# Optimization experiments

Hardware: AMD Instinct MI355X
Metric: run time of the kernel (lower is better)

Reference implementation:

```python
import jax, jax.numpy as jnp
import numpy as np

EPS = float(np.finfo(np.float32).eps)


def fake_quant_w(w):
    # per-output-channel symmetric int8 fake quant; w: (out, in)
    w_d = jax.lax.stop_gradient(w)
    max_abs = jnp.max(jnp.abs(w_d), axis=1, keepdims=True)
    scale = jnp.maximum(max_abs / 127.0, EPS)
    w_q = jnp.clip(jnp.round(w_d / scale), -127, 127)
    return w_q * scale


def woq_linear(x, w, b):
    return x @ fake_quant_w(w).T + b


def setup_inputs() -> dict:
    key = jax.random.key(0)
    ks = jax.random.split(key, 9)
    dim = 1024
    B, S = 2, 2048
    def wmat(k):
        return jax.random.normal(k, (dim, dim), dtype=jnp.float32) * (1.0 / np.sqrt(dim))
    def bvec(k):
        return jax.random.normal(k, (dim,), dtype=jnp.float32) * 0.01
    return {
        "x": jax.random.normal(ks[0], (B, S, dim), dtype=jnp.float32),
        "wq": wmat(ks[1]), "bq": bvec(ks[2]),
        "wk": wmat(ks[3]), "bk": bvec(ks[4]),
        "wv": wmat(ks[5]), "bv": bvec(ks[6]),
        "wp": wmat(ks[7]), "bp": bvec(ks[8]),
    }


def reference(x, wq, bq, wk, bk, wv, bv, wp, bp):
    B, S, C = x.shape
    H = 16
    D = C // H
    scale = D ** -0.5
    # QKV projections with fake-quantized weights -> (B, H, S, D)
    q = woq_linear(x, wq, bq).reshape(B, S, H, D).transpose(0, 2, 1, 3)
    k = woq_linear(x, wk, bk).reshape(B, S, H, D).transpose(0, 2, 1, 3)
    v = woq_linear(x, wv, bv).reshape(B, S, H, D).transpose(0, 2, 1, 3)
    attn = jnp.einsum("bhsd,bhtd->bhst", q, k) * scale  # (B,H,S,S)
    attn = jax.nn.softmax(attn, axis=-1)
    out = jnp.einsum("bhst,bhtd->bhsd", attn, v)
    out = out.transpose(0, 2, 1, 3).reshape(B, S, C)
    return woq_linear(out, wp, bp)
```

## Files before the change

kernel.cpp:

```cpp
#include <hip/hip_runtime.h>
#include <stdint.h>

typedef short bf16x8 __attribute__((ext_vector_type(8)));
typedef float f32x4 __attribute__((ext_vector_type(4)));
typedef uint16_t u16;
typedef uint32_t u32;
typedef u16 u16x4 __attribute__((ext_vector_type(4)));
typedef u32 u32x2 __attribute__((ext_vector_type(2)));
typedef u32 u32x4 __attribute__((ext_vector_type(4)));

#define EPSF 1.1920929e-07f

static __device__ __forceinline__ u16 f2bf(float f) {
  union { float f; uint32_t u; } v; v.f = f;
  return (u16)((v.u + 0x7FFFu + ((v.u >> 16) & 1u)) >> 16);
}
static __device__ __forceinline__ float bf2f(u16 h) {
  union { uint32_t u; float f; } v; v.u = ((uint32_t)h) << 16;
  return v.f;
}
static __device__ __forceinline__ float exp2_fast(float x) {
  return __builtin_amdgcn_exp2f(x);
}
static __device__ __forceinline__ u32 cvt_pk_bf16(float lo, float hi) {
  u32 r;
  asm("v_cvt_pk_bf16_f32 %0, %1, %2" : "=v"(r) : "v"(lo), "v"(hi));
  return r;
}
static __device__ __forceinline__ void gload_lds16(const void* g, void* l) {
  __builtin_amdgcn_global_load_lds(
      (const __attribute__((address_space(1))) void*)g,
      (__attribute__((address_space(3))) void*)l, 16, 0, 0);
}
template <int N>
static __device__ __forceinline__ void vmwait() {
  asm volatile("s_waitcnt vmcnt(%0)" ::"i"(N) : "memory");
}

__global__ __launch_bounds__(256) void prep_kernel(
    const float* __restrict__ wq, const float* __restrict__ wk,
    const float* __restrict__ wv, const float* __restrict__ wp,
    const float* __restrict__ x,
    u16* __restrict__ wout, float* __restrict__ scales, u16* __restrict__ xb) {
  const int t = threadIdx.x;
  if (blockIdx.x < 4096) {
    const int row = blockIdx.x & 1023;
    const int mat = blockIdx.x >> 10;
    const float* W = (mat == 0) ? wq : (mat == 1) ? wk : (mat == 2) ? wv : wp;
    const float4 v = ((const float4*)(W + (size_t)row * 1024))[t];
    float m = fmaxf(fmaxf(fabsf(v.x), fabsf(v.y)), fmaxf(fabsf(v.z), fabsf(v.w)));
#pragma unroll
    for (int off = 1; off < 64; off <<= 1) m = fmaxf(m, __shfl_xor(m, off));
    __shared__ float red[4];
    if ((t & 63) == 0) red[t >> 6] = m;
    __syncthreads();
    m = fmaxf(fmaxf(red[0], red[1]), fmaxf(red[2], red[3]));
    const float scale = fmaxf(m / 127.0f, EPSF);
    float q0 = fminf(fmaxf(rintf(v.x / scale), -127.f), 127.f);
    float q1 = fminf(fmaxf(rintf(v.y / scale), -127.f), 127.f);
    float q2 = fminf(fmaxf(rintf(v.z / scale), -127.f), 127.f);
    float q3 = fminf(fmaxf(rintf(v.w / scale), -127.f), 127.f);
    u16x4 o; o.x = f2bf(q0); o.y = f2bf(q1); o.z = f2bf(q2); o.w = f2bf(q3);
    *(u16x4*)(wout + ((size_t)(mat * 1024 + row)) * 1024 + t * 4) = o;
    if (t == 0) scales[mat * 1024 + row] = scale;
  } else {
    const int i = (blockIdx.x - 4096) * 256 + t;
    const float4 v = ((const float4*)x)[i];
    u16x4 hv;
    hv.x = f2bf(v.x); hv.y = f2bf(v.y); hv.z = f2bf(v.z); hv.w = f2bf(v.w);
    *(u16x4*)(xb + (size_t)i * 4) = hv;
  }
}

template <int MODE, int MR, int NR, int NT, int KT, int LDA>
__global__ __launch_bounds__(512) void gemm_kernel(
    const u16* __restrict__ A, const u16* __restrict__ Bw,
    const float* __restrict__ scales, const float* __restrict__ b0,
    const float* __restrict__ b1, const float* __restrict__ b2,
    u16* __restrict__ qkv, float* __restrict__ outp) {
  constexpr int BM = 2 * MR * 16;
  constexpr int BN = 4 * NR * 16;
  constexpr int OPS = BM / 64 + BN / 64;
  __shared__ u16 As[2][BM * 64];
  __shared__ u16 Bs[2][BN * 64];
  const int tid = threadIdx.x;
  const int w = tid >> 6, l = tid & 63;
  const int per = gridDim.x >> 3;
  const int L = (blockIdx.x & 7) * per + (blockIdx.x >> 3);
  const int tile_n = (L % NT) * BN;
  const int tile_m = (L / NT) * BM;
  const int wm = w >> 2, wn = w & 3;
  const int l15 = l & 15, l4 = l >> 4;
  const int sw = l15 & 7;

  f32x4 acc[MR][NR];
  const f32x4 vzero = {0.f, 0.f, 0.f, 0.f};
#pragma unroll
  for (int m = 0; m < MR; ++m)
#pragma unroll
    for (int n = 0; n < NR; ++n) acc[m][n] = vzero;

  const int r8 = tid >> 3;
  const int g = tid & 7;
  const int gs = g ^ (r8 & 7);
  auto STAGE = [&](int slot, int j) {
    const int kb = j * 64;
    const int kbB = kb & 1023;
#pragma unroll
    for (int i = 0; i < BM / 64; ++i)
      gload_lds16(A + (size_t)(tile_m + i * 64 + r8) * LDA + kb + gs * 8,
                  &As[slot][(i * 64 + r8) * 64 + g * 8]);
#pragma unroll
    for (int i = 0; i < BN / 64; ++i)
      gload_lds16(Bw + (size_t)(tile_n + i * 64 + r8) * 1024 + kbB + gs * 8,
                  &Bs[slot][(i * 64 + r8) * 64 + g * 8]);
  };

  STAGE(0, 0);
  STAGE(1, 1);
  vmwait<OPS>();
  __builtin_amdgcn_s_barrier();

  for (int j = 0; j < KT; ++j) {
    const int cur = j & 1;
#pragma unroll
    for (int ks = 0; ks < 2; ++ks) {
      bf16x8 af[MR], bfv[NR];
      const int sg8 = ((ks * 4 + l4) ^ sw) * 8;
#pragma unroll
      for (int m = 0; m < MR; ++m)
        af[m] = *(const bf16x8*)(&As[cur][(wm * (MR * 16) + m * 16 + l15) * 64 + sg8]);
#pragma unroll
      for (int n = 0; n < NR; ++n)
        bfv[n] = *(const bf16x8*)(&Bs[cur][(wn * (NR * 16) + n * 16 + l15) * 64 + sg8]);
      __builtin_amdgcn_s_setprio(1);
#pragma unroll
      for (int m = 0; m < MR; ++m)
#pragma unroll
        for (int n = 0; n < NR; ++n)
          acc[m][n] = __builtin_amdgcn_mfma_f32_16x16x32_bf16(af[m], bfv[n], acc[m][n], 0, 0, 0);
      __builtin_amdgcn_s_setprio(0);
    }
    __builtin_amdgcn_s_barrier();
    if (j + 2 < KT) {
      STAGE(cur, j + 2);
      vmwait<OPS>();
    } else {
      vmwait<0>();
    }
    __builtin_amdgcn_s_barrier();
  }

#pragma unroll
  for (int m = 0; m < MR; ++m) {
#pragma unroll
    for (int n = 0; n < NR; ++n) {
      const int col = tile_n + wn * (NR * 16) + n * 16 + l15;
      const float sc = scales[col];
      if constexpr (MODE == 0) {
        const int mat = col >> 10, oo = col & 1023;
        const float* bias = (mat == 0) ? b0 : (mat == 1) ? b1 : b2;
        const float bb = bias[oo];
        const int hh = oo >> 6, dd = oo & 63;
        if (mat == 2) {
          const int rowm0 = tile_m + wm * (MR * 16) + m * 16 + l4 * 4;
          const int b = rowm0 >> 11, s = rowm0 & 2047;
          u16x4 pk;
#pragma unroll
          for (int jj = 0; jj < 4; ++jj) pk[jj] = f2bf(acc[m][n][jj] * sc + bb);
          *(u16x4*)(qkv + (size_t)2 * 4194304 +
                    ((size_t)(b * 16 + hh) * 64 + dd) * 2048 + s) = pk;
        } else {
#pragma unroll
          for (int jj = 0; jj < 4; ++jj) {
            const int rowm = tile_m + wm * (MR * 16) + m * 16 + l4 * 4 + jj;
            const int b = rowm >> 11, s = rowm & 2047;
            float y = acc[m][n][jj] * sc + bb;
            if (mat == 0) y *= 0.18033688011112042f;
            qkv[(size_t)mat * 4194304 + ((size_t)(b * 16 + hh) * 2048 + s) * 64 + dd] = f2bf(y);
          }
        }
      } else {
        const float bb = b0[col];
#pragma unroll
        for (int jj = 0; jj < 4; ++jj) {
          const int rowm = tile_m + wm * (MR * 16) + m * 16 + l4 * 4 + jj;
          outp[(size_t)rowm * 1024 + col] = acc[m][n][jj] * sc + bb;
        }
      }
    }
  }
}

__global__ __launch_bounds__(256, 2) void attn_kernel(
    const u16* __restrict__ qg, const u16* __restrict__ kg,
    const u16* __restrict__ vtg, u16* __restrict__ po) {
  __shared__ u16 Kt[2][128 * 64];
  __shared__ u16 Vt[2][64 * 128];
  const int tid = threadIdx.x;
  const int w = tid >> 6, l = tid & 63;
  const int Lb = (blockIdx.x & 7) * 64 + (blockIdx.x >> 3);
  const int bh = Lb >> 4;
  const int qt = Lb & 15;
  const u16* qp = qg + (size_t)bh * 131072;
  const u16* kp = kg + (size_t)bh * 131072;
  const u16* vp = vtg + (size_t)bh * 131072;
  const int qrow0 = qt * 128 + w * 32;
  const int l15 = l & 15, l4 = l >> 4;
  const int sw = l15 & 7;

  auto STAGE = [&](const int slot, const int kt) {
#pragma unroll
    for (int i = 0; i < 4; ++i) {
      const int rk = i * 32 + (tid >> 3);
      gload_lds16(kp + (size_t)(kt + rk) * 64 + (((tid & 7) ^ (rk & 7)) << 3),
                  &Kt[slot][i * 2048 + tid * 8]);
    }
#pragma unroll
    for (int i = 0; i < 4; ++i) {
      const int rv = i * 16 + (tid >> 4);
      gload_lds16(vp + (size_t)rv * 2048 + kt + (((tid & 15) ^ (rv & 7)) << 3),
                  &Vt[slot][i * 2048 + tid * 8]);
    }
  };

  bf16x8 qfr[2][2];
#pragma unroll
  for (int dk = 0; dk < 2; ++dk)
#pragma unroll
    for (int qf = 0; qf < 2; ++qf)
      qfr[dk][qf] =
          *(const bf16x8*)(qp + (size_t)(qrow0 + qf * 16 + l15) * 64 + dk * 32 + l4 * 8);

  const f32x4 vzero = {0.f, 0.f, 0.f, 0.f};
  f32x4 O[4][2];
#pragma unroll
  for (int di = 0; di < 4; ++di)
#pragma unroll
    for (int qf = 0; qf < 2; ++qf) O[di][qf] = vzero;
  float lrun[2] = {0.f, 0.f};

  auto DO_ITER = [&](const int slot, const int j) {
    f32x4 sfr[2][8];
#pragma unroll
    for (int qf = 0; qf < 2; ++qf)
#pragma unroll
      for (int ki = 0; ki < 8; ++ki) sfr[qf][ki] = vzero;
#pragma unroll
    for (int dk = 0; dk < 2; ++dk) {
      bf16x8 kf[8];
#pragma unroll
      for (int ki = 0; ki < 8; ++ki)
        kf[ki] = *(const bf16x8*)(&Kt[slot][(ki * 16 + l15) * 64 + (((dk * 4 + l4) ^ sw) << 3)]);
      __builtin_amdgcn_s_setprio(1);
#pragma unroll
      for (int ki = 0; ki < 8; ++ki)
#pragma unroll
        for (int qf = 0; qf < 2; ++qf)
          sfr[qf][ki] = __builtin_amdgcn_mfma_f32_16x16x32_bf16(kf[ki], qfr[dk][qf], sfr[qf][ki], 0, 0, 0);
      __builtin_amdgcn_s_setprio(0);
    }

#pragma unroll
    for (int half = 0; half < 2; ++half) {
      u32 pw[2][8];
#pragma unroll
      for (int qf = 0; qf < 2; ++qf) {
        float rs = 0.f;
#pragma unroll
        for (int ki = 0; ki < 4; ++ki) {
          const f32x4 s4 = sfr[qf][half * 4 + ki];
          const float p0 = exp2_fast(s4[0]);
          const float p1 = exp2_fast(s4[1]);
          const float p2 = exp2_fast(s4[2]);
          const float p3 = exp2_fast(s4[3]);
          rs += (p0 + p1) + (p2 + p3);
          pw[qf][ki * 2 + 0] = cvt_pk_bf16(p0, p1);
          pw[qf][ki * 2 + 1] = cvt_pk_bf16(p2, p3);
        }
        lrun[qf] += rs;
      }

#pragma unroll
      for (int kkl = 0; kkl < 2; ++kkl) {
        const int c = half * 2 + kkl;
        const u32x4 t0 = {pw[0][kkl * 4 + 0], pw[0][kkl * 4 + 1],
                          pw[0][kkl * 4 + 2], pw[0][kkl * 4 + 3]};
        const u32x4 t1 = {pw[1][kkl * 4 + 0], pw[1][kkl * 4 + 1],
                          pw[1][kkl * 4 + 2], pw[1][kkl * 4 + 3]};
        const bf16x8 pf0 = __builtin_bit_cast(bf16x8, t0);
        const bf16x8 pf1 = __builtin_bit_cast(bf16x8, t1);
        const int o0 = (((c * 4 + (l4 >> 1)) ^ sw) << 3) + (l4 & 1) * 4;
        const int o1 = (((c * 4 + 2 + (l4 >> 1)) ^ sw) << 3) + (l4 & 1) * 4;
        bf16x8 vf[4];
#pragma unroll
        for (int di = 0; di < 4; ++di) {
          const u16* vrow = &Vt[slot][(di * 16 + l15) * 128];
          const u32x2 lo = *(const u32x2*)(vrow + o0);
          const u32x2 hi = *(const u32x2*)(vrow + o1);
          const u32x4 q = {lo.x, lo.y, hi.x, hi.y};
          vf[di] = __builtin_bit_cast(bf16x8, q);
        }
        __builtin_amdgcn_s_setprio(1);
#pragma unroll
        for (int di = 0; di < 4; ++di) {
          O[di][0] = __builtin_amdgcn_mfma_f32_16x16x32_bf16(pf0, vf[di], O[di][0], 0, 0, 0);
          O[di][1] = __builtin_amdgcn_mfma_f32_16x16x32_bf16(pf1, vf[di], O[di][1], 0, 0, 0);
        }
        __builtin_amdgcn_s_setprio(0);
      }
    }

    __builtin_amdgcn_s_barrier();
    if (j + 2 < 16) {
      STAGE(slot, (j + 2) * 128);
      vmwait<8>();
    } else {
      vmwait<0>();
    }
    __builtin_amdgcn_s_barrier();
  };

  STAGE(0, 0);
  STAGE(1, 128);
  vmwait<8>();
  __builtin_amdgcn_s_barrier();

  for (int jp = 0; jp < 8; ++jp) {
    DO_ITER(0, jp * 2);
    DO_ITER(1, jp * 2 + 1);
  }

  const int b = bh >> 4, hh = bh & 15;
#pragma unroll
  for (int qf = 0; qf < 2; ++qf) {
    lrun[qf] += __shfl_xor(lrun[qf], 16);
    lrun[qf] += __shfl_xor(lrun[qf], 32);
  }
#pragma unroll
  for (int qf = 0; qf < 2; ++qf) {
    float lq[4];
#pragma unroll
    for (int jj = 0; jj < 4; ++jj)
      lq[jj] = __builtin_amdgcn_rcpf(__shfl(lrun[qf], l4 * 4 + jj));
#pragma unroll
    for (int di = 0; di < 4; ++di)
#pragma unroll
      for (int jj = 0; jj < 4; ++jj) {
        const float oval = O[di][qf][jj] * lq[jj];
        const int srw = qrow0 + qf * 16 + l4 * 4 + jj;
        const int c = hh * 64 + di * 16 + l15;
        po[((size_t)(b * 2048 + srw)) * 1024 + c] = f2bf(oval);
      }
  }
}

extern "C" void kernel_launch(void* const* d_in, const int* in_sizes, int n_in,
                              void* d_out, int out_size, void* d_ws, size_t ws_size,
                              hipStream_t stream) {
  (void)in_sizes; (void)n_in; (void)out_size; (void)ws_size;
  const float* x  = (const float*)d_in[0];
  const float* wq = (const float*)d_in[1];
  const float* bq = (const float*)d_in[2];
  const float* wk = (const float*)d_in[3];
  const float* bk = (const float*)d_in[4];
  const float* wv = (const float*)d_in[5];
  const float* bv = (const float*)d_in[6];
  const float* wp = (const float*)d_in[7];
  const float* bp = (const float*)d_in[8];

  char* ws = (char*)d_ws;
  u16*   wquant = (u16*)ws;
  float* scales = (float*)(ws + 8388608);
  u16*   xb     = (u16*)(ws + 8404992);
  u16*   po     = xb;
  u16*   qkv    = (u16*)(ws + 25182208);

  prep_kernel<<<dim3(8192), dim3(256), 0, stream>>>(
      wq, wk, wv, wp, x, wquant, scales, xb);
  gemm_kernel<0, 4, 3, 16, 16, 1024><<<dim3(512), dim3(512), 0, stream>>>(
      xb, wquant, scales, bq, bk, bv, qkv, nullptr);
  attn_kernel<<<dim3(512), dim3(256), 0, stream>>>(
      qkv, qkv + 4194304, qkv + 8388608, po);
  gemm_kernel<1, 2, 2, 8, 16, 1024><<<dim3(512), dim3(512), 0, stream>>>(
      po, wquant + 3145728, scales + 3072, bp, nullptr, nullptr, nullptr, (float*)d_out);
}
```

Before: 96.36 us.

## Split attention KV sequence across two wave groups per block with LDS reduction

New measurement: 98.64 us. +2.4%, slower.

```diff
diff --git a/kernel.cpp b/kernel.cpp
--- a/kernel.cpp
+++ b/kernel.cpp
@@ -192,11 +192,11 @@
   }
 }
 
-__global__ __launch_bounds__(256, 2) void attn_kernel(
+__global__ __launch_bounds__(512, 4) void attn_kernel(
     const u16* __restrict__ qg, const u16* __restrict__ kg,
     const u16* __restrict__ vtg, u16* __restrict__ po) {
-  __shared__ u16 Kt[2][128 * 64];
-  __shared__ u16 Vt[2][64 * 128];
+  __shared__ u16 Kt[2][2][64 * 64];
+  __shared__ u16 Vt[2][2][64 * 64];
   const int tid = threadIdx.x;
   const int w = tid >> 6, l = tid & 63;
   const int Lb = (blockIdx.x & 7) * 64 + (blockIdx.x >> 3);
@@ -205,23 +205,19 @@
   const u16* qp = qg + (size_t)bh * 131072;
   const u16* kp = kg + (size_t)bh * 131072;
   const u16* vp = vtg + (size_t)bh * 131072;
-  const int qrow0 = qt * 128 + w * 32;
+  const int wg = w & 3, grp = w >> 2;
+  const int qrow0 = qt * 128 + wg * 32;
   const int l15 = l & 15, l4 = l >> 4;
   const int sw = l15 & 7;
 
-  auto STAGE = [&](const int slot, const int kt) {
-#pragma unroll
-    for (int i = 0; i < 4; ++i) {
-      const int rk = i * 32 + (tid >> 3);
-      gload_lds16(kp + (size_t)(kt + rk) * 64 + (((tid & 7) ^ (rk & 7)) << 3),
-                  &Kt[slot][i * 2048 + tid * 8]);
-    }
-#pragma unroll
-    for (int i = 0; i < 4; ++i) {
-      const int rv = i * 16 + (tid >> 4);
-      gload_lds16(vp + (size_t)rv * 2048 + kt + (((tid & 15) ^ (rv & 7)) << 3),
-                  &Vt[slot][i * 2048 + tid * 8]);
-    }
+  const int sr = tid >> 3, sg = tid & 7;
+  const int gsw = (sg ^ (sr & 7)) << 3;
+  auto STAGE = [&](const int slot, const int j) {
+    const int kA = j * 64, kB = 1024 + j * 64;
+    gload_lds16(kp + (size_t)(kA + sr) * 64 + gsw, &Kt[slot][0][tid * 8]);
+    gload_lds16(vp + (size_t)sr * 2048 + kA + gsw, &Vt[slot][0][tid * 8]);
+    gload_lds16(kp + (size_t)(kB + sr) * 64 + gsw, &Kt[slot][1][tid * 8]);
+    gload_lds16(vp + (size_t)sr * 2048 + kB + gsw, &Vt[slot][1][tid * 8]);
   };
 
   bf16x8 qfr[2][2];
@@ -241,80 +237,79 @@
   float lrun[2] = {0.f, 0.f};
 
   auto DO_ITER = [&](const int slot, const int j) {
-    f32x4 sfr[2][8];
+    const u16* Kb = &Kt[slot][grp][0];
+    const u16* Vb = &Vt[slot][grp][0];
+
+    f32x4 sfr[2][4];
 #pragma unroll
     for (int qf = 0; qf < 2; ++qf)
 #pragma unroll
-      for (int ki = 0; ki < 8; ++ki) sfr[qf][ki] = vzero;
+      for (int ki = 0; ki < 4; ++ki) sfr[qf][ki] = vzero;
 #pragma unroll
     for (int dk = 0; dk < 2; ++dk) {
-      bf16x8 kf[8];
-#pragma unroll
-      for (int ki = 0; ki < 8; ++ki)
-        kf[ki] = *(const bf16x8*)(&Kt[slot][(ki * 16 + l15) * 64 + (((dk * 4 + l4) ^ sw) << 3)]);
+      bf16x8 kf[4];
+#pragma unroll
+      for (int ki = 0; ki < 4; ++ki)
+        kf[ki] = *(const bf16x8*)(Kb + (ki * 16 + l15) * 64 + (((dk * 4 + l4) ^ sw) << 3));
       __builtin_amdgcn_s_setprio(1);
 #pragma unroll
-      for (int ki = 0; ki < 8; ++ki)
+      for (int ki = 0; ki < 4; ++ki)
 #pragma unroll
         for (int qf = 0; qf < 2; ++qf)
           sfr[qf][ki] = __builtin_amdgcn_mfma_f32_16x16x32_bf16(kf[ki], qfr[dk][qf], sfr[qf][ki], 0, 0, 0);
       __builtin_amdgcn_s_setprio(0);
     }
 
-#pragma unroll
-    for (int half = 0; half < 2; ++half) {
-      u32 pw[2][8];
-#pragma unroll
-      for (int qf = 0; qf < 2; ++qf) {
-        float rs = 0.f;
-#pragma unroll
-        for (int ki = 0; ki < 4; ++ki) {
-          const f32x4 s4 = sfr[qf][half * 4 + ki];
-          const float p0 = exp2_fast(s4[0]);
-          const float p1 = exp2_fast(s4[1]);
-          const float p2 = exp2_fast(s4[2]);
-          const float p3 = exp2_fast(s4[3]);
-          rs += (p0 + p1) + (p2 + p3);
-          pw[qf][ki * 2 + 0] = cvt_pk_bf16(p0, p1);
-          pw[qf][ki * 2 + 1] = cvt_pk_bf16(p2, p3);
-        }
-        lrun[qf] += rs;
+    u32 pw[2][8];
+#pragma unroll
+    for (int qf = 0; qf < 2; ++qf) {
+      float rs = 0.f;
+#pragma unroll
+      for (int ki = 0; ki < 4; ++ki) {
+        const f32x4 s4 = sfr[qf][ki];
+        const float p0 = exp2_fast(s4[0]);
+        const float p1 = exp2_fast(s4[1]);
+        const float p2 = exp2_fast(s4[2]);
+        const float p3 = exp2_fast(s4[3]);
+        rs += (p0 + p1) + (p2 + p3);
+        pw[qf][ki * 2 + 0] = cvt_pk_bf16(p0, p1);
+        pw[qf][ki * 2 + 1] = cvt_pk_bf16(p2, p3);
       }
-
-#pragma unroll
-      for (int kkl = 0; kkl < 2; ++kkl) {
-        const int c = half * 2 + kkl;
-        const u32x4 t0 = {pw[0][kkl * 4 + 0], pw[0][kkl * 4 + 1],
-                          pw[0][kkl * 4 + 2], pw[0][kkl * 4 + 3]};
-        const u32x4 t1 = {pw[1][kkl * 4 + 0], pw[1][kkl * 4 + 1],
-                          pw[1][kkl * 4 + 2], pw[1][kkl * 4 + 3]};
-        const bf16x8 pf0 = __builtin_bit_cast(bf16x8, t0);
-        const bf16x8 pf1 = __builtin_bit_cast(bf16x8, t1);
-        const int o0 = (((c * 4 + (l4 >> 1)) ^ sw) << 3) + (l4 & 1) * 4;
-        const int o1 = (((c * 4 + 2 + (l4 >> 1)) ^ sw) << 3) + (l4 & 1) * 4;
-        bf16x8 vf[4];
-#pragma unroll
-        for (int di = 0; di < 4; ++di) {
-          const u16* vrow = &Vt[slot][(di * 16 + l15) * 128];
-          const u32x2 lo = *(const u32x2*)(vrow + o0);
-          const u32x2 hi = *(const u32x2*)(vrow + o1);
-          const u32x4 q = {lo.x, lo.y, hi.x, hi.y};
-          vf[di] = __builtin_bit_cast(bf16x8, q);
-        }
-        __builtin_amdgcn_s_setprio(1);
-#pragma unroll
-        for (int di = 0; di < 4; ++di) {
-          O[di][0] = __builtin_amdgcn_mfma_f32_16x16x32_bf16(pf0, vf[di], O[di][0], 0, 0, 0);
-          O[di][1] = __builtin_amdgcn_mfma_f32_16x16x32_bf16(pf1, vf[di], O[di][1], 0, 0, 0);
-        }
-        __builtin_amdgcn_s_setprio(0);
+      lrun[qf] += rs;
+    }
+
+#pragma unroll
+    for (int kkl = 0; kkl < 2; ++kkl) {
+      const u32x4 t0 = {pw[0][kkl * 4 + 0], pw[0][kkl * 4 + 1],
+                        pw[0][kkl * 4 + 2], pw[0][kkl * 4 + 3]};
+      const u32x4 t1 = {pw[1][kkl * 4 + 0], pw[1][kkl * 4 + 1],
+                        pw[1][kkl * 4 + 2], pw[1][kkl * 4 + 3]};
+      const bf16x8 pf0 = __builtin_bit_cast(bf16x8, t0);
+      const bf16x8 pf1 = __builtin_bit_cast(bf16x8, t1);
+      const int o0 = (((kkl * 4 + (l4 >> 1)) ^ sw) << 3) + (l4 & 1) * 4;
+      const int o1 = (((kkl * 4 + 2 + (l4 >> 1)) ^ sw) << 3) + (l4 & 1) * 4;
+      bf16x8 vf[4];
+#pragma unroll
+      for (int di = 0; di < 4; ++di) {
+        const u16* vrow = Vb + (di * 16 + l15) * 64;
+        const u32x2 lo = *(const u32x2*)(vrow + o0);
+        const u32x2 hi = *(const u32x2*)(vrow + o1);
+        const u32x4 q = {lo.x, lo.y, hi.x, hi.y};
+        vf[di] = __builtin_bit_cast(bf16x8, q);
       }
+      __builtin_amdgcn_s_setprio(1);
+#pragma unroll
+      for (int di = 0; di < 4; ++di) {
+        O[di][0] = __builtin_amdgcn_mfma_f32_16x16x32_bf16(pf0, vf[di], O[di][0], 0, 0, 0);
+        O[di][1] = __builtin_amdgcn_mfma_f32_16x16x32_bf16(pf1, vf[di], O[di][1], 0, 0, 0);
+      }
+      __builtin_amdgcn_s_setprio(0);
     }
 
     __builtin_amdgcn_s_barrier();
     if (j + 2 < 16) {
-      STAGE(slot, (j + 2) * 128);
-      vmwait<8>();
+      STAGE(slot, j + 2);
+      vmwait<4>();
     } else {
       vmwait<0>();
     }
@@ -322,8 +317,8 @@
   };
 
   STAGE(0, 0);
-  STAGE(1, 128);
-  vmwait<8>();
+  STAGE(1, 1);
+  vmwait<4>();
   __builtin_amdgcn_s_barrier();
 
   for (int jp = 0; jp < 8; ++jp) {
@@ -331,27 +326,47 @@
     DO_ITER(1, jp * 2 + 1);
   }
 
-  const int b = bh >> 4, hh = bh & 15;
-#pragma unroll
-  for (int qf = 0; qf < 2; ++qf) {
-    lrun[qf] += __shfl_xor(lrun[qf], 16);
-    lrun[qf] += __shfl_xor(lrun[qf], 32);
-  }
-#pragma unroll
-  for (int qf = 0; qf < 2; ++qf) {
-    float lq[4];
-#pragma unroll
-    for (int jj = 0; jj < 4; ++jj)
-      lq[jj] = __builtin_amdgcn_rcpf(__shfl(lrun[qf], l4 * 4 + jj));
-#pragma unroll
-    for (int di = 0; di < 4; ++di)
-#pragma unroll
-      for (int jj = 0; jj < 4; ++jj) {
-        const float oval = O[di][qf][jj] * lq[jj];
-        const int srw = qrow0 + qf * 16 + l4 * 4 + jj;
-        const int c = hh * 64 + di * 16 + l15;
-        po[((size_t)(b * 2048 + srw)) * 1024 + c] = f2bf(oval);
-      }
+  float* Osh = (float*)&Kt[0][0][0];
+  float* lsh = (float*)&Vt[0][0][0];
+  if (grp == 1) {
+#pragma unroll
+    for (int qf = 0; qf < 2; ++qf) {
+      float* ob = Osh + (wg * 2 + qf) * 1024;
+#pragma unroll
+      for (int di = 0; di < 4; ++di)
+#pragma unroll
+        for (int jj = 0; jj < 4; ++jj)
+          ob[(l4 * 4 + jj) * 64 + di * 16 + l15] = O[di][qf][jj];
+      lsh[(wg * 2 + qf) * 64 + l] = lrun[qf];
+    }
+  }
+  __syncthreads();
+  if (grp == 0) {
+    const int b = bh >> 4, hh = bh & 15;
+#pragma unroll
+    for (int qf = 0; qf < 2; ++qf) {
+      lrun[qf] += lsh[(wg * 2 + qf) * 64 + l];
+      lrun[qf] += __shfl_xor(lrun[qf], 16);
+      lrun[qf] += __shfl_xor(lrun[qf], 32);
+    }
+#pragma unroll
+    for (int qf = 0; qf < 2; ++qf) {
+      float lq[4];
+#pragma unroll
+      for (int jj = 0; jj < 4; ++jj)
+        lq[jj] = __builtin_amdgcn_rcpf(__shfl(lrun[qf], l4 * 4 + jj));
+      const float* ob = Osh + (wg * 2 + qf) * 1024;
+#pragma unroll
+      for (int di = 0; di < 4; ++di)
+#pragma unroll
+        for (int jj = 0; jj < 4; ++jj) {
+          const float oval =
+              (O[di][qf][jj] + ob[(l4 * 4 + jj) * 64 + di * 16 + l15]) * lq[jj];
+          const int srw = qrow0 + qf * 16 + l4 * 4 + jj;
+          const int c = hh * 64 + di * 16 + l15;
+          po[((size_t)(b * 2048 + srw)) * 1024 + c] = f2bf(oval);
+        }
+    }
   }
 }
 
@@ -380,7 +395,7 @@
       wq, wk, wv, wp, x, wquant, scales, xb);
   gemm_kernel<0, 4, 3, 16, 16, 1024><<<dim3(512), dim3(512), 0, stream>>>(
       xb, wquant, scales, bq, bk, bv, qkv, nullptr);
-  attn_kernel<<<dim3(512), dim3(256), 0, stream>>>(
+  attn_kernel<<<dim3(512), dim3(512), 0, stream>>>(
       qkv, qkv + 4194304, qkv + 8388608, po);
   gemm_kernel<1, 2, 2, 8, 16, 1024><<<dim3(512), dim3(512), 0, stream>>>(
       po, wquant + 3145728, scales + 3072, bp, nullptr, nullptr, nullptr, (float*)d_out);
```
